# Optimization experiments

Measured on AMD Instinct MI355X. Metric: run time of the kernel, lower is better.

Reference implementation:

```python
import jax, jax.numpy as jnp
import numpy as np

B, T, E, H = 4, 2048, 1024, 16
D = E // H  # head_dim = 64


def _rope_tables(seq_len, head_dim):
    # Matches torch: inv_freq over even indices, emb = cat(freqs, freqs)
    inv_freq = 1.0 / (10000.0 ** (np.arange(0, head_dim, 2, dtype=np.float32) / head_dim))
    t = np.arange(seq_len, dtype=np.float32)
    freqs = np.outer(t, inv_freq)            # [T, D/2]
    emb = np.concatenate([freqs, freqs], -1)  # [T, D]
    return jnp.asarray(np.cos(emb)), jnp.asarray(np.sin(emb))


def _apply_rope(x, cos, sin):
    # x: [B, H, T, D]; cos/sin: [T, D] -- replicates the pairwise view in the torch code
    d = x.shape[-1]
    xp = x.reshape(*x.shape[:-1], d // 2, 2)
    c = cos.reshape(cos.shape[0], d // 2, 2)  # broadcast over B,H
    s = sin.reshape(sin.shape[0], d // 2, 2)
    x1, x2 = xp[..., 0], xp[..., 1]
    out = jnp.stack((x1 * c[..., 0] - x2 * s[..., 0],
                     x2 * c[..., 1] + x1 * s[..., 1]), axis=-1)
    return out.reshape(x.shape)


def setup_inputs() -> dict:
    key = jax.random.key(0)
    k1, k2, k3 = jax.random.split(key, 3)
    x = jax.random.normal(k1, (B, T, E), dtype=jnp.float32)
    w_attn = jax.random.normal(k2, (3 * E, E), dtype=jnp.float32) * 0.02
    w_proj = jax.random.normal(k3, (E, E), dtype=jnp.float32) * 0.02
    return {"x": x, "w_attn": w_attn, "w_proj": w_proj}


def reference(x, w_attn, w_proj):
    b, t, e = x.shape
    qkv = x @ w_attn.T                              # [B, T, 3E] (torch Linear: x @ W^T)
    q, k, v = jnp.split(qkv, 3, axis=-1)
    q = q.reshape(b, t, H, D).transpose(0, 2, 1, 3)  # [B, H, T, D]
    k = k.reshape(b, t, H, D).transpose(0, 2, 1, 3)
    v = v.reshape(b, t, H, D).transpose(0, 2, 1, 3)
    cos, sin = _rope_tables(t, D)
    q = _apply_rope(q, cos, sin)
    k = _apply_rope(k, cos, sin)
    scale = 1.0 / jnp.sqrt(jnp.float32(D))
    scores = jnp.einsum("bhqd,bhkd->bhqk", q, k) * scale
    causal = jnp.tril(jnp.ones((t, t), dtype=bool))
    scores = jnp.where(causal, scores, jnp.finfo(scores.dtype).min)
    attn = jax.nn.softmax(scores, axis=-1)
    y = jnp.einsum("bhqk,bhkd->bhqd", attn, v)       # [B, H, T, D]
    y = y.transpose(0, 2, 1, 3).reshape(b, t, e)
    return y @ w_proj.T
```

## Files before the change

kernel.cpp:

```cpp
#include <hip/hip_runtime.h>
#include <hip/hip_bf16.h>

#define TB 2048
#define NH 16
#define HD 64
#define NE 1024
#define NB 4
#define BHD (NB * NH)
#define MTOK (NB * TB)

typedef __attribute__((ext_vector_type(8))) short short8;
typedef __attribute__((ext_vector_type(4))) float f32x4;
typedef __attribute__((ext_vector_type(16))) float f32x16;
typedef __attribute__((ext_vector_type(4))) unsigned int u32x4;

static __device__ __forceinline__ unsigned short f2bf(float f) {
  __hip_bfloat16 h = __float2bfloat16(f);
  return __builtin_bit_cast(unsigned short, h);
}

#define GLDS(g, l)                                                              \
  __builtin_amdgcn_global_load_lds((const __attribute__((address_space(1))) void*)(g), \
                                   (__attribute__((address_space(3))) void*)(l), 16, 0, 0)

__global__ __launch_bounds__(256) void cvt_kernel(const float* __restrict__ in,
                                                  unsigned short* __restrict__ out,
                                                  int n4) {
  int i = blockIdx.x * blockDim.x + threadIdx.x;
  if (i >= n4) return;
  float4 v = reinterpret_cast<const float4*>(in)[i];
  ushort4 o;
  o.x = f2bf(v.x); o.y = f2bf(v.y); o.z = f2bf(v.z); o.w = f2bf(v.w);
  reinterpret_cast<ushort4*>(out)[i] = o;
}

__global__ __launch_bounds__(256) void rope_tab_kernel(float2* __restrict__ tab) {
  int i = blockIdx.x * 256 + threadIdx.x;
  int t = i >> 5, j = i & 31;
  float ang = (float)t * __builtin_exp2f(-(float)j * 0.41524101186092029f);
  float sv, cv;
  sincosf(ang, &sv, &cv);
  tab[i] = make_float2(cv, sv);
}

template <int EPI, int BMW, int BNW>
__global__ __launch_bounds__(BMW * BNW * 64) void gemm_bt(
    const unsigned short* __restrict__ Am, const unsigned short* __restrict__ Bm,
    float* __restrict__ Cout, unsigned short* __restrict__ Qo,
    unsigned short* __restrict__ Ko, unsigned short* __restrict__ Vt,
    const float2* __restrict__ Tab, int Mdim, int Ndim, int Kdim) {
  static_assert(BNW == 2, "wr/wc decode assumes BNW==2");
  constexpr int T = BMW * BNW * 64;
  constexpr int BM = BMW * 64;
  constexpr int BN = BNW * 64;
  __shared__ unsigned short As[BM * 64];
  __shared__ unsigned short Bs[BN * 64];

  const int tid = threadIdx.x;
  const int lane = tid & 63;
  const int w = tid >> 6;
  const int wr = w >> 1;
  const int wc = w & 1;

  const int nwg = gridDim.x * gridDim.y;
  int bid = blockIdx.y * gridDim.x + blockIdx.x;
  const int cpx = nwg >> 3;
  bid = (bid & 7) * cpx + (bid >> 3);
  const int m0 = (bid / gridDim.x) * BM;
  const int n0 = (bid % gridDim.x) * BN;

  const int col16 = lane & 15;
  const int seg = lane >> 4;

  f32x4 acc[4][4];
#pragma unroll
  for (int i = 0; i < 4; ++i)
#pragma unroll
    for (int j = 0; j < 4; ++j) acc[i][j] = f32x4{0.f, 0.f, 0.f, 0.f};

  for (int kt = 0; kt < Kdim; kt += 64) {
#pragma unroll
    for (int i_ = 0; i_ < (BM * 8) / T; ++i_) {
      const int s = i_ * T + tid;
      const int row = s >> 3;
      const int sc = (s & 7) ^ (row & 7);
      GLDS(Am + (size_t)(m0 + row) * Kdim + kt + sc * 8,
           As + (size_t)(i_ * T + (w << 6)) * 8);
    }
#pragma unroll
    for (int i_ = 0; i_ < (BN * 8) / T; ++i_) {
      const int s = i_ * T + tid;
      const int row = s >> 3;
      const int sc = (s & 7) ^ (row & 7);
      GLDS(Bm + (size_t)(n0 + row) * Kdim + kt + sc * 8,
           Bs + (size_t)(i_ * T + (w << 6)) * 8);
    }
    __syncthreads();
#pragma unroll
    for (int kk = 0; kk < 2; ++kk) {
      short8 af[4], bfr[4];
#pragma unroll
      for (int mi = 0; mi < 4; ++mi) {
        const int row = wr * 64 + mi * 16 + col16;
        const int ch = (kk * 4 + seg) ^ (row & 7);
        af[mi] = *reinterpret_cast<const short8*>(
            reinterpret_cast<const char*>(As) + row * 128 + ch * 16);
      }
#pragma unroll
      for (int ni = 0; ni < 4; ++ni) {
        const int row = wc * 64 + ni * 16 + col16;
        const int ch = (kk * 4 + seg) ^ (row & 7);
        bfr[ni] = *reinterpret_cast<const short8*>(
            reinterpret_cast<const char*>(Bs) + row * 128 + ch * 16);
      }
#pragma unroll
      for (int mi = 0; mi < 4; ++mi)
#pragma unroll
        for (int ni = 0; ni < 4; ++ni)
          acc[mi][ni] = __builtin_amdgcn_mfma_f32_16x16x32_bf16(af[mi], bfr[ni],
                                                                acc[mi][ni], 0, 0, 0);
    }
    __syncthreads();
  }

  if (EPI == 0) {
#pragma unroll
    for (int mi = 0; mi < 4; ++mi)
#pragma unroll
      for (int ni = 0; ni < 4; ++ni) {
        const int gn = n0 + wc * 64 + ni * 16 + col16;
#pragma unroll
        for (int r = 0; r < 4; ++r) {
          const int gm = m0 + wr * 64 + mi * 16 + seg * 4 + r;
          Cout[(size_t)gm * Ndim + gn] = acc[mi][ni][r];
        }
      }
  } else {
    const int sec = n0 >> 10;
    const int cbase = (n0 & 1023) + wc * 64;
    const int h = cbase >> 6;
#pragma unroll
    for (int mi = 0; mi < 4; ++mi)
#pragma unroll
      for (int ni = 0; ni < 4; ++ni) {
        const int d = ni * 16 + col16;
        if (sec == 2) {
          const int gm0 = m0 + wr * 64 + mi * 16 + seg * 4;
          const int b = gm0 >> 11;
          const int t0 = gm0 & 2047;
          ushort4 pv;
          pv.x = f2bf(acc[mi][ni][0]);
          pv.y = f2bf(acc[mi][ni][1]);
          pv.z = f2bf(acc[mi][ni][2]);
          pv.w = f2bf(acc[mi][ni][3]);
          const size_t vaddr = (size_t)(b * NH + h) * TB * HD + (size_t)(t0 >> 5) * 2048 +
                               ((d >> 5) * 2 + ((t0 & 31) >> 4)) * 512 +
                               ((t0 >> 3) & 1) * 256 + (d & 31) * 8 + (t0 & 7);
          *reinterpret_cast<ushort4*>(Vt + vaddr) = pv;
        } else {
          const float sgn = (d & 1) ? 1.f : -1.f;
          const int j = d & 31;
#pragma unroll
          for (int r = 0; r < 4; ++r) {
            const int gm = m0 + wr * 64 + mi * 16 + seg * 4 + r;
            const int b = gm >> 11;
            const int t = gm & 2047;
            const float v = acc[mi][ni][r];
            const float p = __shfl_xor(v, 1);
            const float2 csv = Tab[t * 32 + j];
            float rot = v * csv.x + sgn * p * csv.y;
            if (sec == 0) {
              rot *= 0.18033688011112042f;
              Qo[((size_t)(b * NH + h) * TB + t) * HD + d] = f2bf(rot);
            } else {
              const size_t kaddr = (size_t)(b * NH + h) * TB * HD +
                                   (size_t)(t >> 5) * 2048 + (d >> 4) * 512 +
                                   ((d >> 3) & 1) * 256 + (t & 31) * 8 + (d & 7);
              Ko[kaddr] = f2bf(rot);
            }
          }
        }
      }
  }
}

__global__ __launch_bounds__(256) void attn_kernel(
    const unsigned short* __restrict__ Q, const unsigned short* __restrict__ K2,
    const unsigned short* __restrict__ V2, unsigned short* __restrict__ Ao) {
  const int tid = threadIdx.x;
  const int lane = tid & 63;
  const int w = tid >> 6;
  const int bx = blockIdx.x;
  const int qt = 63 - (bx >> 4);
  const int bh = ((bx & 15) << 2) | w;
  const int q0 = qt << 5;
  const int l31 = lane & 31;
  const int hi = lane >> 5;
  const int qm = l31 - 4 * hi;

  const unsigned short* Qb = Q + (size_t)bh * TB * HD;
  const unsigned short* K2b = K2 + (size_t)bh * TB * HD;
  const unsigned short* V2b = V2 + (size_t)bh * TB * HD;
  const int fo = hi * 256 + l31 * 8;

  const int batch = bh >> 4;
  const int h = bh & 15;

#define MASKDIAG(st)                                                            \
  { _Pragma("unroll") for (int r = 0; r < 16; ++r) {                            \
      const int rowb = (r & 3) + 8 * (r >> 2);                                  \
      if (rowb > qm) st[r] = -1e30f; } }

#define PVTILE(st, V0, V1, V2x, V3)                                             \
  {                                                                             \
    unsigned int wd[8];                                                         \
    _Pragma("unroll") for (int i = 0; i < 8; ++i) {                             \
      unsigned int t_;                                                          \
      asm("v_cvt_pk_bf16_f32 %0, %1, %2"                                        \
          : "=v"(t_) : "v"(st[2 * i]), "v"(st[2 * i + 1]));                     \
      wd[i] = t_;                                                               \
    }                                                                           \
    asm("v_permlane32_swap_b32 %0, %1" : "+v"(wd[0]), "+v"(wd[2]));             \
    asm("v_permlane32_swap_b32 %0, %1" : "+v"(wd[1]), "+v"(wd[3]));             \
    asm("v_permlane32_swap_b32 %0, %1" : "+v"(wd[4]), "+v"(wd[6]));             \
    asm("v_permlane32_swap_b32 %0, %1" : "+v"(wd[5]), "+v"(wd[7]));             \
    u32x4 f0 = {wd[0], wd[1], wd[2], wd[3]};                                    \
    u32x4 f1 = {wd[4], wd[5], wd[6], wd[7]};                                    \
    short8 p0 = __builtin_bit_cast(short8, f0);                                 \
    short8 p1 = __builtin_bit_cast(short8, f1);                                 \
    __builtin_amdgcn_s_setprio(1);                                              \
    o0 = __builtin_amdgcn_mfma_f32_32x32x16_bf16(V0, p0, o0, 0, 0, 0);          \
    o1 = __builtin_amdgcn_mfma_f32_32x32x16_bf16(V1, p0, o1, 0, 0, 0);          \
    o0 = __builtin_amdgcn_mfma_f32_32x32x16_bf16(V2x, p1, o0, 0, 0, 0);         \
    o1 = __builtin_amdgcn_mfma_f32_32x32x16_bf16(V3, p1, o1, 0, 0, 0);          \
    __builtin_amdgcn_s_setprio(0);                                              \
  }

  short8 qf[4];
#pragma unroll
  for (int s = 0; s < 4; ++s)
    qf[s] = *reinterpret_cast<const short8*>(
        Qb + (size_t)(q0 + l31) * HD + hi * 8 + s * 16);

  f32x16 o0, o1;
#pragma unroll
  for (int r = 0; r < 16; ++r) { o0[r] = 0.f; o1[r] = 0.f; }
  float mrow = -1e30f, lsum = 0.f;

  short8 kf0[4], kf1[4];
#pragma unroll
  for (int s = 0; s < 4; ++s)
    kf0[s] = *reinterpret_cast<const short8*>(K2b + s * 512 + fo);
  if (q0 >= 32)
#pragma unroll
    for (int s = 0; s < 4; ++s)
      kf1[s] = *reinterpret_cast<const short8*>(K2b + 2048 + s * 512 + fo);

  const int LI = qt >> 1;
  for (int kt = 0; kt <= LI; ++kt) {
    const int kv0 = kt << 6;
    const bool two = (kv0 + 32 <= q0);

    f32x16 s0, s1;
#pragma unroll
    for (int r = 0; r < 16; ++r) { s0[r] = 0.f; s1[r] = 0.f; }
    __builtin_amdgcn_s_setprio(1);
#pragma unroll
    for (int s = 0; s < 4; ++s)
      s0 = __builtin_amdgcn_mfma_f32_32x32x16_bf16(kf0[s], qf[s], s0, 0, 0, 0);
    if (two)
#pragma unroll
      for (int s = 0; s < 4; ++s)
        s1 = __builtin_amdgcn_mfma_f32_32x32x16_bf16(kf1[s], qf[s], s1, 0, 0, 0);
    __builtin_amdgcn_s_setprio(0);

    const unsigned short* Va = V2b + (size_t)(2 * kt) * 2048 + fo;
    short8 va0 = *reinterpret_cast<const short8*>(Va);
    short8 va1 = *reinterpret_cast<const short8*>(Va + 1024);
    short8 va2 = *reinterpret_cast<const short8*>(Va + 512);
    short8 va3 = *reinterpret_cast<const short8*>(Va + 1536);
    short8 vb0, vb1, vb2, vb3;
    if (two) {
      const unsigned short* Vbp = Va + 2048;
      vb0 = *reinterpret_cast<const short8*>(Vbp);
      vb1 = *reinterpret_cast<const short8*>(Vbp + 1024);
      vb2 = *reinterpret_cast<const short8*>(Vbp + 512);
      vb3 = *reinterpret_cast<const short8*>(Vbp + 1536);
    }

    if (kt < LI) {
      const unsigned short* Kn = K2b + (size_t)(2 * kt + 2) * 2048;
#pragma unroll
      for (int s = 0; s < 4; ++s)
        kf0[s] = *reinterpret_cast<const short8*>(Kn + s * 512 + fo);
      if (kv0 + 96 <= q0)
#pragma unroll
        for (int s = 0; s < 4; ++s)
          kf1[s] = *reinterpret_cast<const short8*>(Kn + 2048 + s * 512 + fo);
    }

    if (kv0 == q0) MASKDIAG(s0);
    if (two && (kv0 + 32 == q0)) MASKDIAG(s1);

    float mx[8];
#pragma unroll
    for (int i = 0; i < 8; ++i) mx[i] = fmaxf(s0[2 * i], s0[2 * i + 1]);
    if (two)
#pragma unroll
      for (int i = 0; i < 8; ++i)
        mx[i] = fmaxf(mx[i], fmaxf(s1[2 * i], s1[2 * i + 1]));
#pragma unroll
    for (int i = 0; i < 4; ++i) mx[i] = fmaxf(mx[i], mx[i + 4]);
    float pm = fmaxf(fmaxf(mx[0], mx[1]), fmaxf(mx[2], mx[3]));
    pm = fmaxf(pm, __shfl_xor(pm, 32));
    if (!__all(pm - mrow <= 8.f)) {
      const float mn = fmaxf(mrow, pm);
      const float fs = __builtin_exp2f(mrow - mn);
      mrow = mn;
      lsum *= fs;
#pragma unroll
      for (int r = 0; r < 16; ++r) { o0[r] *= fs; o1[r] *= fs; }
    }
    float sm[8];
#pragma unroll
    for (int i = 0; i < 8; ++i) {
      s0[2 * i] = __builtin_exp2f(s0[2 * i] - mrow);
      s0[2 * i + 1] = __builtin_exp2f(s0[2 * i + 1] - mrow);
      sm[i] = s0[2 * i] + s0[2 * i + 1];
    }
    if (two)
#pragma unroll
      for (int i = 0; i < 8; ++i) {
        s1[2 * i] = __builtin_exp2f(s1[2 * i] - mrow);
        s1[2 * i + 1] = __builtin_exp2f(s1[2 * i + 1] - mrow);
        sm[i] += s1[2 * i] + s1[2 * i + 1];
      }
#pragma unroll
    for (int i = 0; i < 4; ++i) sm[i] += sm[i + 4];
    float rs = (sm[0] + sm[1]) + (sm[2] + sm[3]);
    rs += __shfl_xor(rs, 32);
    lsum += rs;

    PVTILE(s0, va0, va1, va2, va3);
    if (two) PVTILE(s1, vb0, vb1, vb2, vb3);
  }

  const float inv = 1.f / lsum;
  unsigned short* Aor = Ao + ((size_t)(batch * TB + q0 + l31)) * NE + (h << 6);
#pragma unroll
  for (int dt = 0; dt < 2; ++dt) {
#pragma unroll
    for (int qd = 0; qd < 4; ++qd) {
      ushort4 pk;
      pk.x = f2bf((dt ? o1[4 * qd + 0] : o0[4 * qd + 0]) * inv);
      pk.y = f2bf((dt ? o1[4 * qd + 1] : o0[4 * qd + 1]) * inv);
      pk.z = f2bf((dt ? o1[4 * qd + 2] : o0[4 * qd + 2]) * inv);
      pk.w = f2bf((dt ? o1[4 * qd + 3] : o0[4 * qd + 3]) * inv);
      *reinterpret_cast<ushort4*>(Aor + dt * 32 + 8 * qd + 4 * hi) = pk;
    }
  }
#undef MASKDIAG
#undef PVTILE
}

extern "C" void kernel_launch(void* const* d_in, const int* in_sizes, int n_in,
                              void* d_out, int out_size, void* d_ws, size_t ws_size,
                              hipStream_t stream) {
  const float* x = (const float*)d_in[0];
  const float* w_attn = (const float*)d_in[1];
  const float* w_proj = (const float*)d_in[2];
  float* out = (float*)d_out;
  char* ws = (char*)d_ws;

  const size_t SZ_XB = (size_t)MTOK * NE * 2;
  const size_t SZ_WA = (size_t)3 * NE * NE * 2;
  const size_t SZ_WP = (size_t)NE * NE * 2;
  const size_t SZ_T = (size_t)BHD * TB * HD * 2;

  unsigned short* xb = (unsigned short*)(ws);
  unsigned short* wab = (unsigned short*)(ws + SZ_XB);
  unsigned short* wpb = (unsigned short*)(ws + SZ_XB + SZ_WA);
  unsigned short* Qs = (unsigned short*)(ws + SZ_XB + SZ_WA + SZ_WP);
  unsigned short* K2 = (unsigned short*)(ws + SZ_XB + SZ_WA + SZ_WP + SZ_T);
  unsigned short* V2 = (unsigned short*)(ws + SZ_XB + SZ_WA + SZ_WP + 2 * SZ_T);
  unsigned short* Ao = (unsigned short*)(ws + SZ_XB + SZ_WA + SZ_WP + 3 * SZ_T);
  float2* tab = (float2*)Ao;

  hipLaunchKernelGGL(cvt_kernel, dim3(MTOK * NE / 4 / 256), dim3(256), 0, stream,
                     x, xb, MTOK * NE / 4);
  hipLaunchKernelGGL(cvt_kernel, dim3(3 * NE * NE / 4 / 256), dim3(256), 0, stream,
                     w_attn, wab, 3 * NE * NE / 4);
  hipLaunchKernelGGL(cvt_kernel, dim3(NE * NE / 4 / 256), dim3(256), 0, stream,
                     w_proj, wpb, NE * NE / 4);
  hipLaunchKernelGGL(rope_tab_kernel, dim3(TB * 32 / 256), dim3(256), 0, stream, tab);

  hipLaunchKernelGGL((gemm_bt<1, 4, 2>), dim3(3 * NE / 128, MTOK / 256), dim3(512),
                     0, stream, xb, wab, nullptr, Qs, K2, V2, tab, MTOK, 3 * NE, NE);

  hipLaunchKernelGGL(attn_kernel, dim3(1024), dim3(256), 0, stream,
                     Qs, K2, V2, Ao);

  hipLaunchKernelGGL((gemm_bt<0, 2, 2>), dim3(NE / 128, MTOK / 128), dim3(256),
                     0, stream, Ao, wpb, out, nullptr, nullptr, nullptr,
                     (const float2*)nullptr, MTOK, NE, NE);
}
```

Before: 193.5 us.

## Fuse prep kernels, remap QKV GEMM tile order, enlarge projection GEMM tiles

Merges the three fp32-to-bf16 conversion launches and the RoPE table launch into a single prep kernel that dispatches on block index, cutting launch count and inter-kernel gaps. The QKV GEMM gets a custom block-to-tile mapping that groups tiles per XCD into 4x12 (bm, bn) regions for better L2 reuse. The output projection GEMM switches from 128x128 tiles with 256 threads to 256x128 tiles with 512 threads, which halves its workgroup count and may reduce occupancy or wave balance.

Result: no change. 193.3 us (-0.1%).

```diff
diff --git a/kernel.cpp b/kernel.cpp
--- a/kernel.cpp
+++ b/kernel.cpp
@@ -23,24 +23,31 @@
   __builtin_amdgcn_global_load_lds((const __attribute__((address_space(1))) void*)(g), \
                                    (__attribute__((address_space(3))) void*)(l), 16, 0, 0)
 
-__global__ __launch_bounds__(256) void cvt_kernel(const float* __restrict__ in,
-                                                  unsigned short* __restrict__ out,
-                                                  int n4) {
-  int i = blockIdx.x * blockDim.x + threadIdx.x;
-  if (i >= n4) return;
-  float4 v = reinterpret_cast<const float4*>(in)[i];
-  ushort4 o;
-  o.x = f2bf(v.x); o.y = f2bf(v.y); o.z = f2bf(v.z); o.w = f2bf(v.w);
-  reinterpret_cast<ushort4*>(out)[i] = o;
-}
-
-__global__ __launch_bounds__(256) void rope_tab_kernel(float2* __restrict__ tab) {
-  int i = blockIdx.x * 256 + threadIdx.x;
-  int t = i >> 5, j = i & 31;
-  float ang = (float)t * __builtin_exp2f(-(float)j * 0.41524101186092029f);
-  float sv, cv;
-  sincosf(ang, &sv, &cv);
-  tab[i] = make_float2(cv, sv);
+__global__ __launch_bounds__(256) void prep_kernel(
+    const float* __restrict__ x, const float* __restrict__ wa,
+    const float* __restrict__ wp, unsigned short* __restrict__ xb,
+    unsigned short* __restrict__ wab, unsigned short* __restrict__ wpb,
+    float2* __restrict__ tab) {
+  const int b = blockIdx.x;
+  if (b < 12288) {
+    const float* src;
+    unsigned short* dst;
+    int i;
+    if (b < 8192)      { src = x;  dst = xb;  i = b * 256 + threadIdx.x; }
+    else if (b < 11264){ src = wa; dst = wab; i = (b - 8192) * 256 + threadIdx.x; }
+    else               { src = wp; dst = wpb; i = (b - 11264) * 256 + threadIdx.x; }
+    float4 v = reinterpret_cast<const float4*>(src)[i];
+    ushort4 o;
+    o.x = f2bf(v.x); o.y = f2bf(v.y); o.z = f2bf(v.z); o.w = f2bf(v.w);
+    reinterpret_cast<ushort4*>(dst)[i] = o;
+  } else {
+    const int i = (b - 12288) * 256 + threadIdx.x;
+    const int t = i >> 5, j = i & 31;
+    float ang = (float)t * __builtin_exp2f(-(float)j * 0.41524101186092029f);
+    float sv, cv;
+    sincosf(ang, &sv, &cv);
+    tab[i] = make_float2(cv, sv);
+  }
 }
 
 template <int EPI, int BMW, int BNW>
@@ -62,12 +69,23 @@
   const int wr = w >> 1;
   const int wc = w & 1;
 
-  const int nwg = gridDim.x * gridDim.y;
-  int bid = blockIdx.y * gridDim.x + blockIdx.x;
-  const int cpx = nwg >> 3;
-  bid = (bid & 7) * cpx + (bid >> 3);
-  const int m0 = (bid / gridDim.x) * BM;
-  const int n0 = (bid % gridDim.x) * BN;
+  int bm, bn;
+  {
+    int bid = blockIdx.y * gridDim.x + blockIdx.x;
+    if (EPI == 1) {
+      const int x_ = bid & 7, i_ = bid >> 3;
+      bm = (x_ >> 1) * 8 + i_ / 12;
+      bn = (x_ & 1) * 12 + i_ % 12;
+    } else {
+      const int nwg = gridDim.x * gridDim.y;
+      const int cpx = nwg >> 3;
+      bid = (bid & 7) * cpx + (bid >> 3);
+      bm = bid / gridDim.x;
+      bn = bid % gridDim.x;
+    }
+  }
+  const int m0 = bm * BM;
+  const int n0 = bn * BN;
 
   const int col16 = lane & 15;
   const int seg = lane >> 4;
@@ -386,13 +404,8 @@
   unsigned short* Ao = (unsigned short*)(ws + SZ_XB + SZ_WA + SZ_WP + 3 * SZ_T);
   float2* tab = (float2*)Ao;
 
-  hipLaunchKernelGGL(cvt_kernel, dim3(MTOK * NE / 4 / 256), dim3(256), 0, stream,
-                     x, xb, MTOK * NE / 4);
-  hipLaunchKernelGGL(cvt_kernel, dim3(3 * NE * NE / 4 / 256), dim3(256), 0, stream,
-                     w_attn, wab, 3 * NE * NE / 4);
-  hipLaunchKernelGGL(cvt_kernel, dim3(NE * NE / 4 / 256), dim3(256), 0, stream,
-                     w_proj, wpb, NE * NE / 4);
-  hipLaunchKernelGGL(rope_tab_kernel, dim3(TB * 32 / 256), dim3(256), 0, stream, tab);
+  hipLaunchKernelGGL(prep_kernel, dim3(12544), dim3(256), 0, stream,
+                     x, w_attn, w_proj, xb, wab, wpb, tab);
 
   hipLaunchKernelGGL((gemm_bt<1, 4, 2>), dim3(3 * NE / 128, MTOK / 256), dim3(512),
                      0, stream, xb, wab, nullptr, Qs, K2, V2, tab, MTOK, 3 * NE, NE);
@@ -400,7 +413,7 @@
   hipLaunchKernelGGL(attn_kernel, dim3(1024), dim3(256), 0, stream,
                      Qs, K2, V2, Ao);
 
-  hipLaunchKernelGGL((gemm_bt<0, 2, 2>), dim3(NE / 128, MTOK / 128), dim3(256),
+  hipLaunchKernelGGL((gemm_bt<0, 4, 2>), dim3(NE / 128, MTOK / 256), dim3(512),
                      0, stream, Ao, wpb, out, nullptr, nullptr, nullptr,
                      (const float2*)nullptr, MTOK, NE, NE);
 }
```
